# Performance work log

Hardware: AMD Instinct MI355X
Metric: run time of the kernel (lower is better)

Reference implementation:

```python
import jax, jax.numpy as jnp
import numpy as np

# --- static hash-grid config (matches tcnn HashGrid in the torch module) ---
DIM = 3
N_LEVELS = 16
F = 2                      # n_features_per_level
LOG2_T = 19
T = 1 << LOG2_T            # hashmap size per level
BASE_RES = 16
TARGET_RES = 2048
PLS = float(np.exp2(np.log2(TARGET_RES / BASE_RES) / (N_LEVELS - 1)))  # per_level_scale
SCALES = [BASE_RES * PLS ** l for l in range(N_LEVELS)]
PRIMES = np.array([1, 2654435761, 805459861], dtype=np.uint32)
# 8 corner offsets of the unit cube, shape [8, 3]
OFFS = np.stack(np.meshgrid(*([np.arange(2)] * DIM), indexing='ij'), -1).reshape(-1, DIM).astype(np.float32)


def _hash(idx_u32):
    # idx_u32: [..., 3] uint32 -> [...] uint32 index into table of size T (power of 2)
    h = idx_u32[..., 0] * jnp.uint32(PRIMES[0])
    h = h ^ (idx_u32[..., 1] * jnp.uint32(PRIMES[1]))
    h = h ^ (idx_u32[..., 2] * jnp.uint32(PRIMES[2]))
    return h & jnp.uint32(T - 1)


def hashgrid_encode(x, table):
    # x: [N, 3] in [0,1); table: [L, T, F] fp32
    outs = []
    offs = jnp.asarray(OFFS)                      # [8, 3]
    for l in range(N_LEVELS):
        pos = x * jnp.float32(SCALES[l])          # [N, 3]
        base = jnp.floor(pos)
        frac = pos - base                         # [N, 3]
        corner = base[:, None, :] + offs[None]    # [N, 8, 3]
        idx = corner.astype(jnp.uint32)
        h = _hash(idx)                            # [N, 8]
        feat = table[l][h]                        # [N, 8, F] (gather)
        # trilinear weights: prod over dims of frac or (1-frac)
        w = jnp.prod(jnp.where(offs[None] > 0.5, frac[:, None, :], 1.0 - frac[:, None, :]), axis=-1)  # [N, 8]
        outs.append(jnp.sum(w[..., None] * feat, axis=1))  # [N, F]
    return jnp.concatenate(outs, axis=-1)         # [N, L*F] = [N, 32]


def setup_inputs() -> dict:
    key = jax.random.key(0)
    ks = jax.random.split(key, 8)
    N = 1048576
    dim_in = N_LEVELS * F          # 32
    hid = 16                       # (16+15)//16*16
    dout = 16                      # grid_output_dim
    x = jax.random.uniform(ks[0], (N, DIM), dtype=jnp.float32)
    table = jax.random.uniform(ks[1], (N_LEVELS, T, F), dtype=jnp.float32, minval=-1e-4, maxval=1e-4)
    def lin(k, fi, fo):
        b = 1.0 / np.sqrt(fi)
        return jax.random.uniform(k, (fo, fi), dtype=jnp.float32, minval=-b, maxval=b)
    W0 = lin(ks[2], dim_in, hid); b0 = jnp.zeros((hid,), jnp.float32)
    W1 = lin(ks[3], hid, hid);    b1 = jnp.zeros((hid,), jnp.float32)
    W2 = lin(ks[4], hid, dout);   b2 = jnp.zeros((dout,), jnp.float32)
    return {"x": x, "table": table, "W0": W0, "b0": b0, "W1": W1, "b1": b1, "W2": W2, "b2": b2}


def reference(x, table, W0, b0, W1, b1, W2, b2):
    h = hashgrid_encode(x, table)                 # [N, 32]
    h = jax.nn.relu(h @ W0.T + b0)
    h = jax.nn.relu(h @ W1.T + b1)
    return h @ W2.T + b2                          # [N, 16]
```

## Files before the change

### kernel.cpp

```cpp
#include <hip/hip_runtime.h>
#include <math.h>

#define NLV 16
#define LOG2_T 19
#define T_SIZE (1u << LOG2_T)
#define T_MASK (T_SIZE - 1u)
#define P2 2654435761u
#define P3 805459861u
#define NBUCK 32768

typedef float vf2 __attribute__((ext_vector_type(2)));
typedef float vf4 __attribute__((ext_vector_type(4)));

struct Scales { float s[NLV]; };

__device__ __forceinline__ unsigned mpart(unsigned v) {
    v = (v | (v << 8)) & 0x100Fu;
    v = (v | (v << 4)) & 0x10C3u;
    v = (v | (v << 2)) & 0x1249u;
    return v;
}
__device__ __forceinline__ unsigned mkey(float px, float py, float pz) {
    unsigned cx = (unsigned)(px * 32.f); cx = cx > 31u ? 31u : cx;
    unsigned cy = (unsigned)(py * 32.f); cy = cy > 31u ? 31u : cy;
    unsigned cz = (unsigned)(pz * 32.f); cz = cz > 31u ? 31u : cz;
    return mpart(cx) | (mpart(cy) << 1) | (mpart(cz) << 2);
}

__global__ __launch_bounds__(256) void zero_hist_kernel(unsigned* hist) {
    int i = blockIdx.x * 256 + threadIdx.x;
    if (i < NBUCK) hist[i] = 0u;
}

__global__ __launch_bounds__(256) void hist_kernel(
    const float* __restrict__ x, unsigned* __restrict__ hist, int N)
{
    int i = blockIdx.x * 256 + threadIdx.x;
    if (i >= N) return;
    const float px = x[3 * (size_t)i + 0];
    const float py = x[3 * (size_t)i + 1];
    const float pz = x[3 * (size_t)i + 2];
    atomicAdd(&hist[mkey(px, py, pz)], 1u);
}

__global__ __launch_bounds__(1024) void scan_kernel(unsigned* hist) {
    __shared__ unsigned tot[1024];
    const int t = threadIdx.x;
    const unsigned base = (unsigned)t * 32u;
    unsigned loc[32];
    unsigned s = 0;
    #pragma unroll
    for (int k = 0; k < 32; ++k) { loc[k] = s; s += hist[base + k]; }
    tot[t] = s;
    __syncthreads();
    for (int off = 1; off < 1024; off <<= 1) {
        unsigned u = (t >= off) ? tot[t - off] : 0u;
        __syncthreads();
        tot[t] += u;
        __syncthreads();
    }
    const unsigned excl = tot[t] - s;
    #pragma unroll
    for (int k = 0; k < 32; ++k) hist[base + k] = excl + loc[k];
}

__global__ __launch_bounds__(256) void scatter_kernel(
    const float* __restrict__ x, unsigned* __restrict__ cursor,
    vf4* __restrict__ xs, int* __restrict__ perm, int N)
{
    int i = blockIdx.x * 256 + threadIdx.x;
    if (i >= N) return;
    const float px = x[3 * (size_t)i + 0];
    const float py = x[3 * (size_t)i + 1];
    const float pz = x[3 * (size_t)i + 2];
    const unsigned key = mkey(px, py, pz);
    const unsigned pos = atomicAdd(&cursor[key], 1u);
    vf4 v; v[0] = px; v[1] = py; v[2] = pz; v[3] = 0.f;
    xs[pos] = v;
    perm[pos] = i;
}

__device__ __forceinline__ void enc_level(
    float px, float py, float pz, float s, const float* __restrict__ tl,
    float& f0, float& f1)
{
    const float fx = px * s, fy = py * s, fz = pz * s;
    const float bx = floorf(fx), by = floorf(fy), bz = floorf(fz);
    const float rx = fx - bx, ry = fy - by, rz = fz - bz;
    const unsigned ix0 = (unsigned)bx, iy0 = (unsigned)by, iz0 = (unsigned)bz;
    const unsigned hx0 = ix0,      hx1 = ix0 + 1u;
    const unsigned hy0 = iy0 * P2, hy1 = (iy0 + 1u) * P2;
    const unsigned hz0 = iz0 * P3, hz1 = (iz0 + 1u) * P3;
    const float wx0 = 1.f - rx, wy0 = 1.f - ry, wz0 = 1.f - rz;
    f0 = 0.f; f1 = 0.f;
    #pragma unroll
    for (int c = 0; c < 8; ++c) {
        unsigned h = ((c & 4) ? hx1 : hx0) ^ ((c & 2) ? hy1 : hy0) ^ ((c & 1) ? hz1 : hz0);
        h &= T_MASK;
        const vf2 f = *(const vf2*)(tl + 2u * (size_t)h);
        const float w = ((c & 4) ? rx : wx0) * ((c & 2) ? ry : wy0) * ((c & 1) ? rz : wz0);
        f0 += w * f[0];
        f1 += w * f[1];
    }
}

__global__ __launch_bounds__(256) void encode_coarse_kernel(
    const vf4* __restrict__ xs, const float* __restrict__ table,
    float* __restrict__ enc, int N, Scales sc)
{
    int i = blockIdx.x * 256 + threadIdx.x;
    if (i >= N) return;
    const vf4 p = xs[i];
    #pragma unroll
    for (int l = 0; l < 5; ++l) {
        float f0, f1;
        enc_level(p[0], p[1], p[2], sc.s[l], table + (size_t)l * T_SIZE * 2u, f0, f1);
        vf2 v; v[0] = f0; v[1] = f1;
        __builtin_nontemporal_store(v, (vf2*)(enc + ((size_t)l * N + i) * 2u));
    }
}

__global__ __launch_bounds__(256) void encode_one_kernel(
    const vf4* __restrict__ xs, const float* __restrict__ tl, float s,
    float* __restrict__ encl, int N)
{
    int i = blockIdx.x * 256 + threadIdx.x;
    if (i >= N) return;
    const vf4 p = xs[i];
    float f0, f1;
    enc_level(p[0], p[1], p[2], s, tl, f0, f1);
    vf2 v; v[0] = f0; v[1] = f1;
    __builtin_nontemporal_store(v, (vf2*)(encl + (size_t)i * 2u));
}

__global__ __launch_bounds__(256) void mlp_kernel(
    const float* __restrict__ enc, const int* __restrict__ perm,
    const float* __restrict__ W0, const float* __restrict__ b0,
    const float* __restrict__ W1, const float* __restrict__ b1,
    const float* __restrict__ W2, const float* __restrict__ b2,
    float* __restrict__ out, int N)
{
    int i = blockIdx.x * 256 + threadIdx.x;
    if (i >= N) return;

    float e[32];
    #pragma unroll
    for (int l = 0; l < NLV; ++l) {
        vf2 v = __builtin_nontemporal_load((const vf2*)(enc + ((size_t)l * N + i) * 2u));
        e[2 * l + 0] = v[0];
        e[2 * l + 1] = v[1];
    }

    float a0[16];
    #pragma unroll
    for (int j = 0; j < 16; ++j) {
        float s = b0[j];
        #pragma unroll
        for (int k = 0; k < 32; ++k) s += e[k] * W0[j * 32 + k];
        a0[j] = fmaxf(s, 0.f);
    }
    float a1[16];
    #pragma unroll
    for (int j = 0; j < 16; ++j) {
        float s = b1[j];
        #pragma unroll
        for (int k = 0; k < 16; ++k) s += a0[k] * W1[j * 16 + k];
        a1[j] = fmaxf(s, 0.f);
    }
    float o[16];
    #pragma unroll
    for (int j = 0; j < 16; ++j) {
        float s = b2[j];
        #pragma unroll
        for (int k = 0; k < 16; ++k) s += a1[k] * W2[j * 16 + k];
        o[j] = s;
    }

    float* op = out + 16 * (size_t)perm[i];
    #pragma unroll
    for (int q = 0; q < 4; ++q) {
        vf4 v; v[0] = o[4*q]; v[1] = o[4*q+1]; v[2] = o[4*q+2]; v[3] = o[4*q+3];
        __builtin_nontemporal_store(v, (vf4*)(op + 4 * q));
    }
}

__global__ __launch_bounds__(256) void encode_coarse_unsorted_kernel(
    const float* __restrict__ x, const float* __restrict__ table,
    float* __restrict__ enc, int N, Scales sc)
{
    int i = blockIdx.x * 256 + threadIdx.x;
    if (i >= N) return;
    const float px = x[3 * (size_t)i + 0];
    const float py = x[3 * (size_t)i + 1];
    const float pz = x[3 * (size_t)i + 2];
    #pragma unroll
    for (int l = 0; l < 5; ++l) {
        float f0, f1;
        enc_level(px, py, pz, sc.s[l], table + (size_t)l * T_SIZE * 2u, f0, f1);
        vf2 v; v[0] = f0; v[1] = f1;
        __builtin_nontemporal_store(v, (vf2*)(enc + ((size_t)l * N + i) * 2u));
    }
}
__global__ __launch_bounds__(256) void encode_one_unsorted_kernel(
    const float* __restrict__ x, const float* __restrict__ tl, float s,
    float* __restrict__ encl, int N)
{
    int i = blockIdx.x * 256 + threadIdx.x;
    if (i >= N) return;
    const float px = x[3 * (size_t)i + 0];
    const float py = x[3 * (size_t)i + 1];
    const float pz = x[3 * (size_t)i + 2];
    float f0, f1;
    enc_level(px, py, pz, s, tl, f0, f1);
    vf2 v; v[0] = f0; v[1] = f1;
    __builtin_nontemporal_store(v, (vf2*)(encl + (size_t)i * 2u));
}
__global__ __launch_bounds__(256) void mlp_noperm_kernel(
    const float* __restrict__ enc,
    const float* __restrict__ W0, const float* __restrict__ b0,
    const float* __restrict__ W1, const float* __restrict__ b1,
    const float* __restrict__ W2, const float* __restrict__ b2,
    float* __restrict__ out, int N)
{
    int i = blockIdx.x * 256 + threadIdx.x;
    if (i >= N) return;
    float e[32];
    #pragma unroll
    for (int l = 0; l < NLV; ++l) {
        vf2 v = __builtin_nontemporal_load((const vf2*)(enc + ((size_t)l * N + i) * 2u));
        e[2 * l + 0] = v[0];
        e[2 * l + 1] = v[1];
    }
    float a0[16];
    #pragma unroll
    for (int j = 0; j < 16; ++j) {
        float s = b0[j];
        #pragma unroll
        for (int k = 0; k < 32; ++k) s += e[k] * W0[j * 32 + k];
        a0[j] = fmaxf(s, 0.f);
    }
    float a1[16];
    #pragma unroll
    for (int j = 0; j < 16; ++j) {
        float s = b1[j];
        #pragma unroll
        for (int k = 0; k < 16; ++k) s += a0[k] * W1[j * 16 + k];
        a1[j] = fmaxf(s, 0.f);
    }
    #pragma unroll
    for (int j = 0; j < 16; ++j) {
        float s = b2[j];
        #pragma unroll
        for (int k = 0; k < 16; ++k) s += a1[k] * W2[j * 16 + k];
        out[16 * (size_t)i + j] = s;
    }
}
__global__ __launch_bounds__(256) void tcnn_fused_kernel(
    const float* __restrict__ x, const float* __restrict__ table,
    const float* __restrict__ W0, const float* __restrict__ b0,
    const float* __restrict__ W1, const float* __restrict__ b1,
    const float* __restrict__ W2, const float* __restrict__ b2,
    float* __restrict__ out, int N, Scales sc)
{
    int i = blockIdx.x * blockDim.x + threadIdx.x;
    if (i >= N) return;
    const float px = x[3 * (size_t)i + 0];
    const float py = x[3 * (size_t)i + 1];
    const float pz = x[3 * (size_t)i + 2];
    float e[32];
    #pragma unroll
    for (int l = 0; l < NLV; ++l) {
        float f0, f1;
        enc_level(px, py, pz, sc.s[l], table + (size_t)l * T_SIZE * 2u, f0, f1);
        e[2 * l] = f0; e[2 * l + 1] = f1;
    }
    float a0[16];
    #pragma unroll
    for (int j = 0; j < 16; ++j) {
        float s = b0[j];
        #pragma unroll
        for (int k = 0; k < 32; ++k) s += e[k] * W0[j * 32 + k];
        a0[j] = fmaxf(s, 0.f);
    }
    float a1[16];
    #pragma unroll
    for (int j = 0; j < 16; ++j) {
        float s = b1[j];
        #pragma unroll
        for (int k = 0; k < 16; ++k) s += a0[k] * W1[j * 16 + k];
        a1[j] = fmaxf(s, 0.f);
    }
    #pragma unroll
    for (int j = 0; j < 16; ++j) {
        float s = b2[j];
        #pragma unroll
        for (int k = 0; k < 16; ++k) s += a1[k] * W2[j * 16 + k];
        out[16 * (size_t)i + j] = s;
    }
}

extern "C" void kernel_launch(void* const* d_in, const int* in_sizes, int n_in,
                              void* d_out, int out_size, void* d_ws, size_t ws_size,
                              hipStream_t stream) {
    const float* x     = (const float*)d_in[0];
    const float* table = (const float*)d_in[1];
    const float* W0    = (const float*)d_in[2];
    const float* b0    = (const float*)d_in[3];
    const float* W1    = (const float*)d_in[4];
    const float* b1    = (const float*)d_in[5];
    const float* W2    = (const float*)d_in[6];
    const float* b2    = (const float*)d_in[7];
    float* out = (float*)d_out;

    const int N = in_sizes[0] / 3;

    Scales sc;
    const double pls = exp2(log2(2048.0 / 16.0) / 15.0);
    for (int l = 0; l < NLV; ++l) sc.s[l] = (float)(16.0 * pow(pls, (double)l));

    const int block = 256;
    const int grid = (N + block - 1) / block;

    const size_t encB  = (size_t)N * 2u * NLV * sizeof(float);
    const size_t xsB   = (size_t)N * sizeof(float) * 4u;
    const size_t permB = (size_t)N * sizeof(int);
    const size_t histB = (size_t)NBUCK * sizeof(unsigned);

    if (ws_size >= encB + xsB + permB + histB) {
        float*    enc  = (float*)d_ws;
        vf4*      xs   = (vf4*)((char*)d_ws + encB);
        int*      perm = (int*)((char*)d_ws + encB + xsB);
        unsigned* hist = (unsigned*)((char*)d_ws + encB + xsB + permB);

        zero_hist_kernel<<<(NBUCK + 255) / 256, block, 0, stream>>>(hist);
        hist_kernel<<<grid, block, 0, stream>>>(x, hist, N);
        scan_kernel<<<1, 1024, 0, stream>>>(hist);
        scatter_kernel<<<grid, block, 0, stream>>>(x, hist, xs, perm, N);

        encode_coarse_kernel<<<grid, block, 0, stream>>>(xs, table, enc, N, sc);
        for (int l = 5; l < NLV; ++l) {
            encode_one_kernel<<<grid, block, 0, stream>>>(
                xs, table + (size_t)l * T_SIZE * 2u, sc.s[l],
                enc + (size_t)l * (size_t)N * 2u, N);
        }
        mlp_kernel<<<grid, block, 0, stream>>>(enc, perm, W0, b0, W1, b1, W2, b2, out, N);
    } else if (ws_size >= encB) {
        float* enc = (float*)d_ws;
        encode_coarse_unsorted_kernel<<<grid, block, 0, stream>>>(x, table, enc, N, sc);
        for (int l = 5; l < NLV; ++l) {
            encode_one_unsorted_kernel<<<grid, block, 0, stream>>>(
                x, table + (size_t)l * T_SIZE * 2u, sc.s[l],
                enc + (size_t)l * (size_t)N * 2u, N);
        }
        mlp_noperm_kernel<<<grid, block, 0, stream>>>(enc, W0, b0, W1, b1, W2, b2, out, N);
    } else {
        tcnn_fused_kernel<<<grid, block, 0, stream>>>(x, table, W0, b0, W1, b1, W2, b2,
                                                      out, N, sc);
    }
}
```

Measured before the change: 623.4 us.

## Process two points per thread in fine-level encode and coalesce permuted MLP output

The per-level encode kernel now handles two points per thread with half the grid, giving more independent hash gathers in flight per thread. The MLP kernel stages its 16 outputs in padded shared memory, then writes them back so that four consecutive threads store one 64-byte output row to the permuted destination. This replaces scattered per-thread 64-byte stores with more contiguous ones. Encoded-feature loads drop the nontemporal hint, and the MLP kernel adds a block-wide barrier and extra shared memory that may reduce occupancy.

```diff
diff --git a/kernel.cpp b/kernel.cpp
--- a/kernel.cpp
+++ b/kernel.cpp
@@ -124,13 +124,21 @@
     const vf4* __restrict__ xs, const float* __restrict__ tl, float s,
     float* __restrict__ encl, int N)
 {
-    int i = blockIdx.x * 256 + threadIdx.x;
-    if (i >= N) return;
-    const vf4 p = xs[i];
-    float f0, f1;
-    enc_level(p[0], p[1], p[2], s, tl, f0, f1);
-    vf2 v; v[0] = f0; v[1] = f1;
-    __builtin_nontemporal_store(v, (vf2*)(encl + (size_t)i * 2u));
+    int i0 = blockIdx.x * 512 + threadIdx.x;
+    int i1 = i0 + 256;
+    if (i0 < N) {
+        const vf4 p0 = xs[i0];
+        const vf4 p1 = (i1 < N) ? xs[i1] : p0;
+        float a0, a1, b0v, b1v;
+        enc_level(p0[0], p0[1], p0[2], s, tl, a0, a1);
+        enc_level(p1[0], p1[1], p1[2], s, tl, b0v, b1v);
+        vf2 va; va[0] = a0; va[1] = a1;
+        __builtin_nontemporal_store(va, (vf2*)(encl + (size_t)i0 * 2u));
+        if (i1 < N) {
+            vf2 vb; vb[0] = b0v; vb[1] = b1v;
+            __builtin_nontemporal_store(vb, (vf2*)(encl + (size_t)i1 * 2u));
+        }
+    }
 }
 
 __global__ __launch_bounds__(256) void mlp_kernel(
@@ -140,47 +148,65 @@
     const float* __restrict__ W2, const float* __restrict__ b2,
     float* __restrict__ out, int N)
 {
-    int i = blockIdx.x * 256 + threadIdx.x;
-    if (i >= N) return;
-
-    float e[32];
-    #pragma unroll
-    for (int l = 0; l < NLV; ++l) {
-        vf2 v = __builtin_nontemporal_load((const vf2*)(enc + ((size_t)l * N + i) * 2u));
-        e[2 * l + 0] = v[0];
-        e[2 * l + 1] = v[1];
-    }
-
-    float a0[16];
-    #pragma unroll
-    for (int j = 0; j < 16; ++j) {
-        float s = b0[j];
-        #pragma unroll
-        for (int k = 0; k < 32; ++k) s += e[k] * W0[j * 32 + k];
-        a0[j] = fmaxf(s, 0.f);
-    }
-    float a1[16];
-    #pragma unroll
-    for (int j = 0; j < 16; ++j) {
-        float s = b1[j];
-        #pragma unroll
-        for (int k = 0; k < 16; ++k) s += a0[k] * W1[j * 16 + k];
-        a1[j] = fmaxf(s, 0.f);
-    }
+    __shared__ float st[256 * 17];
+    const int base = blockIdx.x * 256;
+    const int t = threadIdx.x;
+    const int i = base + t;
+
     float o[16];
-    #pragma unroll
-    for (int j = 0; j < 16; ++j) {
-        float s = b2[j];
-        #pragma unroll
-        for (int k = 0; k < 16; ++k) s += a1[k] * W2[j * 16 + k];
-        o[j] = s;
-    }
-
-    float* op = out + 16 * (size_t)perm[i];
+    if (i < N) {
+        float e[32];
+        #pragma unroll
+        for (int l = 0; l < NLV; ++l) {
+            vf2 v = *(const vf2*)(enc + ((size_t)l * N + i) * 2u);
+            e[2 * l + 0] = v[0];
+            e[2 * l + 1] = v[1];
+        }
+        float a0[16];
+        #pragma unroll
+        for (int j = 0; j < 16; ++j) {
+            float s = b0[j];
+            #pragma unroll
+            for (int k = 0; k < 32; ++k) s += e[k] * W0[j * 32 + k];
+            a0[j] = fmaxf(s, 0.f);
+        }
+        float a1[16];
+        #pragma unroll
+        for (int j = 0; j < 16; ++j) {
+            float s = b1[j];
+            #pragma unroll
+            for (int k = 0; k < 16; ++k) s += a0[k] * W1[j * 16 + k];
+            a1[j] = fmaxf(s, 0.f);
+        }
+        #pragma unroll
+        for (int j = 0; j < 16; ++j) {
+            float s = b2[j];
+            #pragma unroll
+            for (int k = 0; k < 16; ++k) s += a1[k] * W2[j * 16 + k];
+            o[j] = s;
+        }
+    } else {
+        #pragma unroll
+        for (int j = 0; j < 16; ++j) o[j] = 0.f;
+    }
+
     #pragma unroll
     for (int q = 0; q < 4; ++q) {
         vf4 v; v[0] = o[4*q]; v[1] = o[4*q+1]; v[2] = o[4*q+2]; v[3] = o[4*q+3];
-        __builtin_nontemporal_store(v, (vf4*)(op + 4 * q));
+        *(vf4*)&st[t * 17 + 4 * q] = v;
+    }
+    __syncthreads();
+
+    const int c = t & 3;
+    #pragma unroll
+    for (int w = 0; w < 4; ++w) {
+        const int p = (t >> 2) + w * 64;
+        const int gi = base + p;
+        if (gi < N) {
+            const int dst = perm[gi];
+            const vf4 v = *(const vf4*)&st[p * 17 + 4 * c];
+            *(vf4*)(out + 16 * (size_t)dst + 4 * c) = v;
+        }
     }
 }
 
@@ -227,7 +253,7 @@
     float e[32];
     #pragma unroll
     for (int l = 0; l < NLV; ++l) {
-        vf2 v = __builtin_nontemporal_load((const vf2*)(enc + ((size_t)l * N + i) * 2u));
+        vf2 v = *(const vf2*)(enc + ((size_t)l * N + i) * 2u);
         e[2 * l + 0] = v[0];
         e[2 * l + 1] = v[1];
     }
@@ -338,8 +364,9 @@
         scatter_kernel<<<grid, block, 0, stream>>>(x, hist, xs, perm, N);
 
         encode_coarse_kernel<<<grid, block, 0, stream>>>(xs, table, enc, N, sc);
+        const int grid2 = (N + 511) / 512;
         for (int l = 5; l < NLV; ++l) {
-            encode_one_kernel<<<grid, block, 0, stream>>>(
+            encode_one_kernel<<<grid2, block, 0, stream>>>(
                 xs, table + (size_t)l * T_SIZE * 2u, sc.s[l],
                 enc + (size_t)l * (size_t)N * 2u, N);
         }
```

New measurement: 545.8 us. 1.14x faster.
